# Performance work log

Hardware: AMD Instinct MI355X
Metric: run time of the kernel (lower is better)

## Reference

```python
import jax, jax.numpy as jnp
import numpy as np

B = 128          # batch size
N_KG = 500       # KG vertices
N = N_KG + 2     # + sensor node + zero target node
D = 1024         # embed_dim (hard-coded in forward)
H = 256          # gnn_hidden
E = 4000         # edges
EPS = 1e-5


def setup_inputs() -> dict:
    key = jax.random.key(0)
    ks = jax.random.split(key, 8)
    return {
        "sensor_batch": jax.random.normal(ks[0], (B, D), jnp.float32),
        "base_vertices": jax.random.normal(ks[1], (N_KG, D), jnp.float32),
        "edge_index": jax.random.randint(ks[2], (2, E), 0, N, jnp.int64),
        "W1": jax.random.normal(ks[3], (D, H), jnp.float32) * (1.0 / np.sqrt(D)),
        "b1": jnp.zeros((H,), jnp.float32),
        "gamma1": jnp.ones((H,), jnp.float32),
        "beta1": jnp.zeros((H,), jnp.float32),
        "W2": jax.random.normal(ks[4], (H, H), jnp.float32) * (1.0 / np.sqrt(H)),
        "b2": jnp.zeros((H,), jnp.float32),
        "gamma2": jnp.ones((H,), jnp.float32),
        "beta2": jnp.zeros((H,), jnp.float32),
        "W3": jax.random.normal(ks[5], (H, H), jnp.float32) * (1.0 / np.sqrt(H)),
        "b3": jnp.zeros((H,), jnp.float32),
        "gamma3": jnp.ones((H,), jnp.float32),
        "beta3": jnp.zeros((H,), jnp.float32),
    }


def _gcn_norm(edge_index):
    # add self loops, symmetric normalization D^{-1/2} A D^{-1/2}
    loops = jnp.arange(N, dtype=edge_index.dtype)
    src = jnp.concatenate([edge_index[0], loops])
    dst = jnp.concatenate([edge_index[1], loops])
    deg = jnp.zeros((N,), jnp.float32).at[dst].add(1.0)
    dinv = jnp.where(deg > 0, jax.lax.rsqrt(deg), 0.0)
    norm = dinv[src] * dinv[dst]   # [E+N]
    return src, dst, norm


def _gcn_conv(x, W, b, src, dst, norm):
    # x: [B, N, F_in] -> [B, N, F_out]
    h = jnp.einsum('bnf,fh->bnh', x, W)
    msg = h[:, src, :] * norm[None, :, None]            # gather + scale
    out = jnp.zeros_like(h).at[:, dst, :].add(msg)      # scatter-add
    return out + b


def _bn_elu(x, gamma, beta):
    # BatchNorm1d over flattened (B*N, H) in training mode, then ELU
    Bn, Nn, Hh = x.shape
    xf = x.reshape(Bn * Nn, Hh)
    mean = jnp.mean(xf, axis=0)
    var = jnp.mean(jnp.square(xf - mean), axis=0)  # biased, as in torch BN fwd
    y = (xf - mean) * jax.lax.rsqrt(var + EPS) * gamma + beta
    return jax.nn.elu(y).reshape(Bn, Nn, Hh)


def reference(sensor_batch, base_vertices, edge_index,
              W1, b1, gamma1, beta1,
              W2, b2, gamma2, beta2,
              W3, b3, gamma3, beta3):
    Bn = sensor_batch.shape[0]
    # x = [base_vertices; sensor_input; zeros] per batch element -> [B, N, D]
    base = jnp.broadcast_to(base_vertices[None], (Bn, N_KG, D))
    zeros = jnp.zeros((Bn, 1, D), sensor_batch.dtype)
    x = jnp.concatenate([base, sensor_batch[:, None, :], zeros], axis=1)

    src, dst, norm = _gcn_norm(edge_index)
    x = _bn_elu(_gcn_conv(x, W1, b1, src, dst, norm), gamma1, beta1)
    x = _bn_elu(_gcn_conv(x, W2, b2, src, dst, norm), gamma2, beta2)
    x = _bn_elu(_gcn_conv(x, W3, b3, src, dst, norm), gamma3, beta3)
    return x
```

## Files before the change

kernel.cpp:

```cpp
#include <hip/hip_runtime.h>
#include <cstdint>
#include <cstddef>

#define NNODES 502
#define NKG    500
#define NPAD   512
#define NEDGE  4000
#define NET    4502
#define BB     128
#define DD     1024
#define HH     256
#define MROWS  (BB*NNODES)
#define MT     65536
#define MCAT   628

typedef short short8 __attribute__((ext_vector_type(8)));
typedef float f32x4  __attribute__((ext_vector_type(4)));

__device__ __forceinline__ unsigned short f2bf(float f) {
  union { float f; unsigned int u; } v; v.f = f;
  unsigned int r = v.u + 0x7fffu + ((v.u >> 16) & 1u);
  return (unsigned short)(r >> 16);
}

__device__ __forceinline__ float elu(float y) {
  return (y > 0.f) ? y : (__expf(y) - 1.f);
}

__device__ __forceinline__ void stage16(const void* g, void* l) {
  __builtin_amdgcn_global_load_lds((__attribute__((address_space(1))) void*)g,
                                   (__attribute__((address_space(3))) void*)l, 16, 0, 0);
}

__device__ __forceinline__ void mfma16(f32x4& c, short8 a, short8 b) {
  asm volatile("v_mfma_f32_16x16x32_bf16 %0, %1, %2, %0" : "+v"(c) : "v"(a), "v"(b));
}

__device__ inline void get_edge(const int* __restrict__ e, int i, int i64mode,
                                int& src, int& dst) {
  if (i < NEDGE) {
    if (i64mode) { src = e[2*i]; dst = e[2*NEDGE + 2*i]; }
    else         { src = e[i];   dst = e[NEDGE + i]; }
  } else {
    src = dst = i - NEDGE;
  }
  src = min(max(src, 0), NNODES-1);
  dst = min(max(dst, 0), NNODES-1);
}

__global__ void detect_kernel(const int* __restrict__ e, int* __restrict__ flag) {
  int v = e[2*threadIdx.x + 1];
  if (v != 0) atomicOr(flag, 1);
}

__global__ void deg_kernel(const int* __restrict__ e, const int* __restrict__ flag,
                           int* __restrict__ deg) {
  int i = blockIdx.x*256 + threadIdx.x;
  if (i >= NET) return;
  int src, dst; get_edge(e, i, *flag == 0, src, dst);
  atomicAdd(&deg[dst], 1);
}

__global__ void scan_kernel(const int* __restrict__ deg, float* __restrict__ dinv,
                            int* __restrict__ rp, int* __restrict__ cursor) {
  __shared__ int s[512];
  int t = threadIdx.x;
  int cnt = (t < NNODES) ? deg[t] : 0;
  s[t] = cnt;
  if (t < NNODES) dinv[t] = rsqrtf((float)cnt);
  __syncthreads();
  for (int off = 1; off < 512; off <<= 1) {
    int v = (t >= off) ? s[t-off] : 0;
    __syncthreads();
    s[t] += v;
    __syncthreads();
  }
  if (t == 0) rp[0] = 0;
  if (t < NNODES) { rp[t+1] = s[t]; cursor[t] = s[t] - cnt; }
}

__global__ void fill_kernel(const int* __restrict__ e, const int* __restrict__ flag,
                            const float* __restrict__ dinv, int* __restrict__ cursor,
                            int* __restrict__ colA, float* __restrict__ valA) {
  int i = blockIdx.x*256 + threadIdx.x;
  if (i >= NET) return;
  int src, dst; get_edge(e, i, *flag == 0, src, dst);
  int pos = atomicAdd(&cursor[dst], 1);
  colA[pos] = src;
  valA[pos] = dinv[src] * dinv[dst];
}

__global__ void sdf_kernel(const int* __restrict__ e, const int* __restrict__ flag,
                           const float* __restrict__ dinv, float* __restrict__ Sdf) {
  int i = blockIdx.x*256 + threadIdx.x;
  if (i >= NET) return;
  int src, dst; get_edge(e, i, *flag == 0, src, dst);
  atomicAdd(&Sdf[dst*NPAD + src], dinv[src]*dinv[dst]);
}

__global__ void sdcvt_kernel(const float* __restrict__ Sdf, unsigned short* __restrict__ Sd) {
  int i = blockIdx.x*256 + threadIdx.x;
  Sd[i] = f2bf(Sdf[i]);
}

__global__ __launch_bounds__(256) void prep_kernel(
    const float* __restrict__ W1, const float* __restrict__ W2, const float* __restrict__ W3,
    const float* __restrict__ base, const float* __restrict__ sensor,
    unsigned short* __restrict__ Wt1, unsigned short* __restrict__ Wt2,
    unsigned short* __restrict__ Wt3, unsigned short* __restrict__ Xp1) {
  int bid = blockIdx.x, tid = threadIdx.x;
  if (bid < 512) {
    const float* W = (bid & 256) ? W3 : W2;
    unsigned short* Wt = (bid & 256) ? Wt3 : Wt2;
    int n = bid & 255;
    Wt[n*HH + tid] = f2bf(W[(size_t)tid*HH + n]);
  } else if (bid < 768) {
    int n = bid - 512;
    for (int k = tid; k < DD; k += 256)
      Wt1[n*DD + k] = f2bf(W1[(size_t)k*HH + n]);
  } else {
    int i = (bid - 768)*256 + tid;
    int r = i >> 8, c = (i & 255) * 4;
    float4 v = make_float4(0.f, 0.f, 0.f, 0.f);
    if (r < NKG) v = *(const float4*)&base[(size_t)r*DD + c];
    else if (r < MCAT) v = *(const float4*)&sensor[(size_t)(r-NKG)*DD + c];
    union { unsigned short u[4]; uint2 d; } p;
    p.u[0]=f2bf(v.x); p.u[1]=f2bf(v.y); p.u[2]=f2bf(v.z); p.u[3]=f2bf(v.w);
    *(uint2*)&Xp1[(size_t)r*DD + c] = p.d;
  }
}

__global__ __launch_bounds__(256) void gemm1m_kernel(
    const unsigned short* __restrict__ Ag,
    const unsigned short* __restrict__ Bg,
    float* __restrict__ C) {
  __shared__ unsigned short As[128*32];
  __shared__ unsigned short Bs[128*32];
  int tid = threadIdx.x;
  int wave = tid >> 6, lane = tid & 63;
  int l15 = lane & 15, quad = lane >> 4;
  int wm = (wave & 1) * 64, wn = (wave >> 1) * 64;
  int row0 = blockIdx.y * 128, col0 = blockIdx.x * 128;
  f32x4 acc[4][4] = {};
  for (int k0 = 0; k0 < DD; k0 += 32) {
#pragma unroll
    for (int q = 0; q < 2; ++q) {
      int c = wave*128 + q*64 + lane;
      stage16(Ag + (size_t)(row0 + (c>>2))*DD + k0 + (c&3)*8, As + c*8);
      stage16(Bg + (size_t)(col0 + (c>>2))*DD + k0 + (c&3)*8, Bs + c*8);
    }
    __syncthreads();
    short8 af[4], bfv[4];
#pragma unroll
    for (int i = 0; i < 4; ++i) {
      af[i]  = *(const short8*)(As + (wm + i*16 + l15)*32 + quad*8);
      bfv[i] = *(const short8*)(Bs + (wn + i*16 + l15)*32 + quad*8);
    }
#pragma unroll
    for (int mi = 0; mi < 4; ++mi)
#pragma unroll
      for (int ni = 0; ni < 4; ++ni)
        mfma16(acc[mi][ni], af[mi], bfv[ni]);
    __syncthreads();
  }
  asm volatile("s_nop 7\n\ts_nop 7" ::);
#pragma unroll
  for (int ni = 0; ni < 4; ++ni) {
    int n = col0 + wn + ni*16 + l15;
#pragma unroll
    for (int mi = 0; mi < 4; ++mi) {
      int m = row0 + wm + mi*16 + quad*4;
#pragma unroll
      for (int r = 0; r < 4; ++r)
        if (m + r < MCAT) C[(size_t)(m+r)*HH + n] = acc[mi][ni][r];
    }
  }
}

__global__ void ac_kernel(const int* __restrict__ rp, const int* __restrict__ colA,
                          const float* __restrict__ valA, const float* __restrict__ hcat,
                          float* __restrict__ Abuf, float* __restrict__ cbuf) {
  int n = blockIdx.x, h = threadIdx.x;
  int s = rp[n], e = rp[n+1];
  float acc = 0.f, cacc = 0.f;
  for (int t = s; t < e; ++t) {
    int cl = colA[t]; float v = valA[t];
    if (cl < NKG) acc += v * hcat[cl*HH + h];
    else if (cl == NKG) cacc += v;
  }
  Abuf[n*HH + h] = acc;
  if (h == 0) cbuf[n] = cacc;
}

__global__ __launch_bounds__(256) void bn1n_kernel(
    const float* __restrict__ Abuf, const float* __restrict__ cbuf,
    const float* __restrict__ hcat,
    float* __restrict__ sA1, float* __restrict__ sAA1, float* __restrict__ sAc1,
    float* __restrict__ scp, float* __restrict__ ssA, float* __restrict__ sssA) {
  int bid = blockIdx.x, h = threadIdx.x;
  if (bid < 32) {
    int n0 = bid*16, n1 = min(n0+16, NNODES);
    float sA = 0, sAA = 0, sAc = 0, sc = 0, scc = 0;
    for (int n = n0; n < n1; ++n) {
      float a = Abuf[n*HH + h]; float cn = cbuf[n];
      sA += a; sAA += a*a; sAc += a*cn; sc += cn; scc += cn*cn;
    }
    atomicAdd(&sA1[h], sA); atomicAdd(&sAA1[h], sAA); atomicAdd(&sAc1[h], sAc);
    if (h == 0) { atomicAdd(&scp[0], sc); atomicAdd(&scp[1], scc); }
  } else {
    int b0 = (bid-32)*16;
    float ss = 0, sss = 0;
    for (int b = b0; b < b0+16; ++b) {
      float v = hcat[(size_t)(NKG + b)*HH + h]; ss += v; sss += v*v;
    }
    atomicAdd(&ssA[h], ss); atomicAdd(&sssA[h], sss);
  }
}

__global__ void fin1_kernel(const float* __restrict__ sA1, const float* __restrict__ sAA1,
                            const float* __restrict__ sAc1, const float* __restrict__ scp,
                            const float* __restrict__ ssA, const float* __restrict__ sssA,
                            const float* __restrict__ gamma, const float* __restrict__ beta,
                            float* __restrict__ scale, float* __restrict__ shift) {
  int h = threadIdx.x;
  float sA = sA1[h], sAA = sAA1[h], sAc = sAc1[h];
  float sc = scp[0], scc = scp[1];
  float ss = ssA[h], sss = sssA[h];
  const float cnt = (float)MROWS;
  float mean = ((float)BB * sA + sc*ss) / cnt;
  float msq  = ((float)BB * sAA + 2.f*sAc*ss + scc*sss) / cnt;
  float var  = msq - mean*mean;
  float scl  = gamma[h] * rsqrtf(var + 1e-5f);
  scale[h] = scl; shift[h] = beta[h] - mean*scl;
}

__global__ __launch_bounds__(256) void x2_kernel(
    const float* __restrict__ Abuf, const float* __restrict__ cbuf,
    const float* __restrict__ hcat, const float* __restrict__ scale,
    const float* __restrict__ shift, unsigned short* __restrict__ Xb) {
  int idx = blockIdx.x*256 + threadIdx.x;
  int row = idx >> 6, h0 = (idx & 63)*4;
  int b = row >> 9, n = row & (NPAD-1);
  union { unsigned short u[4]; uint2 d; } p;
  p.d = make_uint2(0,0);
  if (n < NNODES) {
    float4 a  = *(const float4*)(Abuf + n*HH + h0);
    float4 s  = *(const float4*)(hcat + (size_t)(NKG + b)*HH + h0);
    float4 sc = *(const float4*)(scale + h0);
    float4 sh = *(const float4*)(shift + h0);
    float cn = cbuf[n];
    p.u[0] = f2bf(elu((a.x + cn*s.x)*sc.x + sh.x));
    p.u[1] = f2bf(elu((a.y + cn*s.y)*sc.y + sh.y));
    p.u[2] = f2bf(elu((a.z + cn*s.z)*sc.z + sh.z));
    p.u[3] = f2bf(elu((a.w + cn*s.w)*sc.w + sh.w));
  }
  *(uint2*)(Xb + (size_t)row*HH + h0) = p.d;
}

__global__ __launch_bounds__(256) void gemmT_kernel(
    const unsigned short* __restrict__ Ag,
    const unsigned short* __restrict__ Bg,
    unsigned short* __restrict__ Tt) {
  __shared__ unsigned short As[128*32];
  __shared__ unsigned short Bs[128*32];
  int tid = threadIdx.x;
  int wave = tid >> 6, lane = tid & 63;
  int l15 = lane & 15, quad = lane >> 4;
  int wm = (wave & 1) * 64, wn = (wave >> 1) * 64;
  int row0 = blockIdx.y * 128, col0 = blockIdx.x * 128;
  f32x4 acc[4][4] = {};
  for (int k0 = 0; k0 < HH; k0 += 32) {
#pragma unroll
    for (int q = 0; q < 2; ++q) {
      int c = wave*128 + q*64 + lane;
      stage16(Ag + (size_t)(row0 + (c>>2))*HH + k0 + (c&3)*8, As + c*8);
      stage16(Bg + (size_t)(col0 + (c>>2))*HH + k0 + (c&3)*8, Bs + c*8);
    }
    __syncthreads();
    short8 af[4], bfv[4];
#pragma unroll
    for (int i = 0; i < 4; ++i) {
      af[i]  = *(const short8*)(As + (wm + i*16 + l15)*32 + quad*8);
      bfv[i] = *(const short8*)(Bs + (wn + i*16 + l15)*32 + quad*8);
    }
#pragma unroll
    for (int mi = 0; mi < 4; ++mi)
#pragma unroll
      for (int ni = 0; ni < 4; ++ni)
        mfma16(acc[mi][ni], af[mi], bfv[ni]);
    __syncthreads();
  }
  asm volatile("s_nop 7\n\ts_nop 7" ::);
#pragma unroll
  for (int ni = 0; ni < 4; ++ni) {
    int n = col0 + wn + ni*16 + l15;
#pragma unroll
    for (int mi = 0; mi < 4; ++mi) {
      int m = row0 + wm + mi*16 + quad*4;
      union { unsigned short u[4]; uint2 v; } p;
#pragma unroll
      for (int r = 0; r < 4; ++r) p.u[r] = f2bf(acc[mi][ni][r]);
      *(uint2*)(Tt + (size_t)n*MT + m) = p.v;
    }
  }
}

__global__ __launch_bounds__(256) void gemmS_kernel(
    const unsigned short* __restrict__ Sd,
    const unsigned short* __restrict__ Tt,
    float* __restrict__ O,
    float* __restrict__ sums, float* __restrict__ ssqs) {
  __shared__ unsigned short As[128*32];
  __shared__ unsigned short Bs[128*32];
  int tid = threadIdx.x;
  int wave = tid >> 6, lane = tid & 63;
  int l15 = lane & 15, quad = lane >> 4;
  int wm = (wave & 1) * 64, wn = (wave >> 1) * 64;
  int row0 = blockIdx.y * 128, col0 = blockIdx.x * 128;
  int b = blockIdx.z;
  f32x4 acc[4][4] = {};
  for (int k0 = 0; k0 < NPAD; k0 += 32) {
#pragma unroll
    for (int q = 0; q < 2; ++q) {
      int c = wave*128 + q*64 + lane;
      stage16(Sd + (size_t)(row0 + (c>>2))*NPAD + k0 + (c&3)*8, As + c*8);
      stage16(Tt + (size_t)(col0 + (c>>2))*MT + b*NPAD + k0 + (c&3)*8, Bs + c*8);
    }
    __syncthreads();
    short8 af[4], bfv[4];
#pragma unroll
    for (int i = 0; i < 4; ++i) {
      af[i]  = *(const short8*)(As + (wm + i*16 + l15)*32 + quad*8);
      bfv[i] = *(const short8*)(Bs + (wn + i*16 + l15)*32 + quad*8);
    }
#pragma unroll
    for (int mi = 0; mi < 4; ++mi)
#pragma unroll
      for (int ni = 0; ni < 4; ++ni)
        mfma16(acc[mi][ni], af[mi], bfv[ni]);
    __syncthreads();
  }
  asm volatile("s_nop 7\n\ts_nop 7" ::);
  float* Ob = O + (size_t)b*NNODES*HH;
  float ps[4] = {0,0,0,0}, pq[4] = {0,0,0,0};
#pragma unroll
  for (int ni = 0; ni < 4; ++ni) {
    int n = col0 + wn + ni*16 + l15;
#pragma unroll
    for (int mi = 0; mi < 4; ++mi) {
      int node = row0 + wm + mi*16 + quad*4;
#pragma unroll
      for (int r = 0; r < 4; ++r) {
        float v = acc[mi][ni][r];
        if (node + r < NNODES) Ob[(size_t)(node+r)*HH + n] = v;
        ps[ni] += v; pq[ni] += v*v;
      }
    }
  }
  __syncthreads();
  float* red = (float*)As;
  red[tid] = 0.f;
  __syncthreads();
#pragma unroll
  for (int ni = 0; ni < 4; ++ni) {
    int cl = wn + ni*16 + l15;
    atomicAdd(&red[cl], ps[ni]);
    atomicAdd(&red[128+cl], pq[ni]);
  }
  __syncthreads();
  if (tid < 128) atomicAdd(&sums[col0+tid], red[tid]);
  else atomicAdd(&ssqs[col0+tid-128], red[tid]);
}

__global__ void finalize_kernel(const float* __restrict__ sums, const float* __restrict__ ssqs,
                                const float* __restrict__ gamma, const float* __restrict__ beta,
                                float* __restrict__ scale, float* __restrict__ shift) {
  int h = threadIdx.x;
  const float cnt = (float)MROWS;
  float mean = sums[h] / cnt;
  float var  = ssqs[h] / cnt - mean*mean;
  float scl  = gamma[h] * rsqrtf(var + 1e-5f);
  scale[h] = scl; shift[h] = beta[h] - mean*scl;
}

__global__ __launch_bounds__(256) void bnxb_kernel(
    const float* __restrict__ O, const float* __restrict__ scale,
    const float* __restrict__ shift, unsigned short* __restrict__ Xb) {
  int idx = blockIdx.x*256 + threadIdx.x;
  int row = idx >> 6, h0 = (idx & 63)*4;
  int b = row >> 9, n = row & (NPAD-1);
  union { unsigned short u[4]; uint2 d; } p;
  p.d = make_uint2(0,0);
  if (n < NNODES) {
    float4 v  = *(const float4*)(O + ((size_t)(b*NNODES + n)*HH + h0));
    float4 sc = *(const float4*)(scale + h0);
    float4 sh = *(const float4*)(shift + h0);
    p.u[0] = f2bf(elu(v.x*sc.x + sh.x));
    p.u[1] = f2bf(elu(v.y*sc.y + sh.y));
    p.u[2] = f2bf(elu(v.z*sc.z + sh.z));
    p.u[3] = f2bf(elu(v.w*sc.w + sh.w));
  }
  *(uint2*)(Xb + (size_t)row*HH + h0) = p.d;
}

__global__ __launch_bounds__(256) void bnout_kernel(
    float* __restrict__ O, const float* __restrict__ scale,
    const float* __restrict__ shift) {
  int i = blockIdx.x*256 + threadIdx.x;
  int h0 = (i & 63)*4;
  float4 v = *(float4*)(O + (size_t)i*4);
  float4 sc = *(const float4*)(scale + h0);
  float4 sh = *(const float4*)(shift + h0);
  v.x = elu(v.x*sc.x + sh.x);
  v.y = elu(v.y*sc.y + sh.y);
  v.z = elu(v.z*sc.z + sh.z);
  v.w = elu(v.w*sc.w + sh.w);
  *(float4*)(O + (size_t)i*4) = v;
}

extern "C" void kernel_launch(void* const* d_in, const int* in_sizes, int n_in,
                              void* d_out, int out_size, void* d_ws, size_t ws_size,
                              hipStream_t stream) {
  const float* sensor = (const float*)d_in[0];
  const float* base   = (const float*)d_in[1];
  const int*   eidx   = (const int*)d_in[2];
  const float* W1 = (const float*)d_in[3];
  const float* g1 = (const float*)d_in[5];
  const float* be1= (const float*)d_in[6];
  const float* W2 = (const float*)d_in[7];
  const float* g2 = (const float*)d_in[9];
  const float* be2= (const float*)d_in[10];
  const float* W3 = (const float*)d_in[11];
  const float* g3 = (const float*)d_in[13];
  const float* be3= (const float*)d_in[14];

  char* ws = (char*)d_ws;
  int*   deg    = (int*)(ws + 0);
  float* sum2   = (float*)(ws + 2048);
  float* ssq2   = (float*)(ws + 3072);
  float* sum3   = (float*)(ws + 4096);
  float* ssq3   = (float*)(ws + 5120);
  float* cbuf   = (float*)(ws + 6144);
  int*   cursor = (int*)(ws + 8192);
  int*   flag   = (int*)(ws + 10240);
  float* sA1    = (float*)(ws + 10496);
  float* sAA1   = (float*)(ws + 11520);
  float* sAc1   = (float*)(ws + 12544);
  float* scp    = (float*)(ws + 13568);
  float* ssA    = (float*)(ws + 13824);
  float* sssA   = (float*)(ws + 14848);
  float* dinv   = (float*)(ws + 16384);
  int*   rp     = (int*)(ws + 18432);
  int*   colA   = (int*)(ws + 20480);
  float* valA   = (float*)(ws + 40960);
  float* scale1 = (float*)(ws + 61440);
  float* shift1 = (float*)(ws + 62464);
  float* scale2 = (float*)(ws + 63488);
  float* shift2 = (float*)(ws + 64512);
  float* scale3 = (float*)(ws + 65536);
  float* shift3 = (float*)(ws + 66560);
  float* Abuf   = (float*)(ws + 67584);
  float* hcat   = (float*)(ws + 581632);
  unsigned short* Wt2 = (unsigned short*)(ws + 1224704);
  unsigned short* Wt3 = (unsigned short*)(ws + 1355776);
  unsigned short* Sd  = (unsigned short*)(ws + 1486848);
  unsigned short* Xb  = (unsigned short*)(ws + 2011136);
  unsigned short* Tt  = (unsigned short*)(ws + 35565568UL);
  unsigned short* Xp1 = (unsigned short*)(ws + 35565568UL);
  unsigned short* Wt1 = (unsigned short*)(ws + 35565568UL + 1310720);
  float* out = (float*)d_out;
  float* Sdf = (float*)d_out;

  hipMemsetAsync(ws, 0, 16384, stream);
  hipMemsetAsync(d_out, 0, NPAD*NPAD*4, stream);
  detect_kernel<<<1, 256, 0, stream>>>(eidx, flag);
  deg_kernel<<<(NET+255)/256, 256, 0, stream>>>(eidx, flag, deg);
  scan_kernel<<<1, 512, 0, stream>>>(deg, dinv, rp, cursor);
  fill_kernel<<<(NET+255)/256, 256, 0, stream>>>(eidx, flag, dinv, cursor, colA, valA);
  sdf_kernel<<<(NET+255)/256, 256, 0, stream>>>(eidx, flag, dinv, Sdf);
  sdcvt_kernel<<<(NPAD*NPAD)/256, 256, 0, stream>>>(Sdf, Sd);
  prep_kernel<<<1408, 256, 0, stream>>>(W1, W2, W3, base, sensor, Wt1, Wt2, Wt3, Xp1);

  gemm1m_kernel<<<dim3(2, 5), 256, 0, stream>>>(Xp1, Wt1, hcat);
  ac_kernel<<<NNODES, 256, 0, stream>>>(rp, colA, valA, hcat, Abuf, cbuf);
  bn1n_kernel<<<40, 256, 0, stream>>>(Abuf, cbuf, hcat, sA1, sAA1, sAc1, scp, ssA, sssA);
  fin1_kernel<<<1, 256, 0, stream>>>(sA1, sAA1, sAc1, scp, ssA, sssA, g1, be1, scale1, shift1);
  x2_kernel<<<(MT*64)/256, 256, 0, stream>>>(Abuf, cbuf, hcat, scale1, shift1, Xb);

  gemmT_kernel<<<dim3(2, MT/128), 256, 0, stream>>>(Xb, Wt2, Tt);
  gemmS_kernel<<<dim3(2, 4, BB), 256, 0, stream>>>(Sd, Tt, out, sum2, ssq2);
  finalize_kernel<<<1, 256, 0, stream>>>(sum2, ssq2, g2, be2, scale2, shift2);
  bnxb_kernel<<<(MT*64)/256, 256, 0, stream>>>(out, scale2, shift2, Xb);

  gemmT_kernel<<<dim3(2, MT/128), 256, 0, stream>>>(Xb, Wt3, Tt);
  gemmS_kernel<<<dim3(2, 4, BB), 256, 0, stream>>>(Sd, Tt, out, sum3, ssq3);
  finalize_kernel<<<1, 256, 0, stream>>>(sum3, ssq3, g3, be3, scale3, shift3);
  bnout_kernel<<<(MROWS*64)/256, 256, 0, stream>>>(out, scale3, shift3);
}
```

Before: 334.5 us.

## Store aggregation GEMM output as bf16 in place and remap blocks across XCDs

The aggregation GEMM now writes its result as bf16 straight into the activation buffer instead of fp32 into the output. BN+ELU then runs in place on that bf16 buffer, and the final layer converts from bf16 to fp32 output in one pass. This cuts intermediate fp32 traffic. The grid is also flattened to 1D with an XCD-aware index remap so blocks sharing a batch land on the same XCD cache. In exchange, pre-BN values are rounded to bf16 before normalization, which adds some precision loss in the final layer's output.

```diff
diff --git a/kernel.cpp b/kernel.cpp
--- a/kernel.cpp
+++ b/kernel.cpp
@@ -21,6 +21,11 @@
   union { float f; unsigned int u; } v; v.f = f;
   unsigned int r = v.u + 0x7fffu + ((v.u >> 16) & 1u);
   return (unsigned short)(r >> 16);
+}
+
+__device__ __forceinline__ float bf2f(unsigned short u) {
+  union { unsigned int u; float f; } v; v.u = ((unsigned int)u) << 16;
+  return v.f;
 }
 
 __device__ __forceinline__ float elu(float y) {
@@ -308,7 +313,7 @@
 __global__ __launch_bounds__(256) void gemmS_kernel(
     const unsigned short* __restrict__ Sd,
     const unsigned short* __restrict__ Tt,
-    float* __restrict__ O,
+    unsigned short* __restrict__ Xbo,
     float* __restrict__ sums, float* __restrict__ ssqs) {
   __shared__ unsigned short As[128*32];
   __shared__ unsigned short Bs[128*32];
@@ -316,8 +321,14 @@
   int wave = tid >> 6, lane = tid & 63;
   int l15 = lane & 15, quad = lane >> 4;
   int wm = (wave & 1) * 64, wn = (wave >> 1) * 64;
-  int row0 = blockIdx.y * 128, col0 = blockIdx.x * 128;
-  int b = blockIdx.z;
+  int id = blockIdx.x;
+  int xcd = id & 7;
+  int w = id >> 3;
+  int y = w & 3;
+  int g = (w >> 2) * 8 + xcd;
+  int x = g >> 7;
+  int b = g & 127;
+  int row0 = y * 128, col0 = x * 128;
   f32x4 acc[4][4] = {};
   for (int k0 = 0; k0 < NPAD; k0 += 32) {
 #pragma unroll
@@ -341,7 +352,7 @@
     __syncthreads();
   }
   asm volatile("s_nop 7\n\ts_nop 7" ::);
-  float* Ob = O + (size_t)b*NNODES*HH;
+  unsigned short* Xrow = Xbo + (size_t)b*NPAD*HH;
   float ps[4] = {0,0,0,0}, pq[4] = {0,0,0,0};
 #pragma unroll
   for (int ni = 0; ni < 4; ++ni) {
@@ -352,7 +363,7 @@
 #pragma unroll
       for (int r = 0; r < 4; ++r) {
         float v = acc[mi][ni][r];
-        if (node + r < NNODES) Ob[(size_t)(node+r)*HH + n] = v;
+        if (node + r < NNODES) Xrow[(size_t)(node+r)*HH + n] = f2bf(v);
         ps[ni] += v; pq[ni] += v*v;
       }
     }
@@ -383,39 +394,42 @@
   scale[h] = scl; shift[h] = beta[h] - mean*scl;
 }
 
-__global__ __launch_bounds__(256) void bnxb_kernel(
-    const float* __restrict__ O, const float* __restrict__ scale,
-    const float* __restrict__ shift, unsigned short* __restrict__ Xb) {
+__global__ __launch_bounds__(256) void bnip_kernel(
+    unsigned short* __restrict__ Xb, const float* __restrict__ scale,
+    const float* __restrict__ shift) {
+  int idx = blockIdx.x*256 + threadIdx.x;
+  int row = idx >> 6, h0 = (idx & 63)*4;
+  int n = row & (NPAD-1);
+  if (n >= NNODES) return;
+  unsigned short* p = Xb + (size_t)row*HH + h0;
+  union { unsigned short u[4]; uint2 d; } v;
+  v.d = *(uint2*)p;
+  float4 sc = *(const float4*)(scale + h0);
+  float4 sh = *(const float4*)(shift + h0);
+  v.u[0] = f2bf(elu(bf2f(v.u[0])*sc.x + sh.x));
+  v.u[1] = f2bf(elu(bf2f(v.u[1])*sc.y + sh.y));
+  v.u[2] = f2bf(elu(bf2f(v.u[2])*sc.z + sh.z));
+  v.u[3] = f2bf(elu(bf2f(v.u[3])*sc.w + sh.w));
+  *(uint2*)p = v.d;
+}
+
+__global__ __launch_bounds__(256) void bnout_kernel(
+    const unsigned short* __restrict__ Xb, const float* __restrict__ scale,
+    const float* __restrict__ shift, float* __restrict__ O) {
   int idx = blockIdx.x*256 + threadIdx.x;
   int row = idx >> 6, h0 = (idx & 63)*4;
   int b = row >> 9, n = row & (NPAD-1);
-  union { unsigned short u[4]; uint2 d; } p;
-  p.d = make_uint2(0,0);
-  if (n < NNODES) {
-    float4 v  = *(const float4*)(O + ((size_t)(b*NNODES + n)*HH + h0));
-    float4 sc = *(const float4*)(scale + h0);
-    float4 sh = *(const float4*)(shift + h0);
-    p.u[0] = f2bf(elu(v.x*sc.x + sh.x));
-    p.u[1] = f2bf(elu(v.y*sc.y + sh.y));
-    p.u[2] = f2bf(elu(v.z*sc.z + sh.z));
-    p.u[3] = f2bf(elu(v.w*sc.w + sh.w));
-  }
-  *(uint2*)(Xb + (size_t)row*HH + h0) = p.d;
-}
-
-__global__ __launch_bounds__(256) void bnout_kernel(
-    float* __restrict__ O, const float* __restrict__ scale,
-    const float* __restrict__ shift) {
-  int i = blockIdx.x*256 + threadIdx.x;
-  int h0 = (i & 63)*4;
-  float4 v = *(float4*)(O + (size_t)i*4);
+  if (n >= NNODES) return;
+  union { unsigned short u[4]; uint2 d; } v;
+  v.d = *(const uint2*)(Xb + (size_t)row*HH + h0);
   float4 sc = *(const float4*)(scale + h0);
   float4 sh = *(const float4*)(shift + h0);
-  v.x = elu(v.x*sc.x + sh.x);
-  v.y = elu(v.y*sc.y + sh.y);
-  v.z = elu(v.z*sc.z + sh.z);
-  v.w = elu(v.w*sc.w + sh.w);
-  *(float4*)(O + (size_t)i*4) = v;
+  float4 o;
+  o.x = elu(bf2f(v.u[0])*sc.x + sh.x);
+  o.y = elu(bf2f(v.u[1])*sc.y + sh.y);
+  o.z = elu(bf2f(v.u[2])*sc.z + sh.z);
+  o.w = elu(bf2f(v.u[3])*sc.w + sh.w);
+  *(float4*)(O + ((size_t)(b*NNODES + n)*HH + h0)) = o;
 }
 
 extern "C" void kernel_launch(void* const* d_in, const int* in_sizes, int n_in,
@@ -488,12 +502,12 @@
   x2_kernel<<<(MT*64)/256, 256, 0, stream>>>(Abuf, cbuf, hcat, scale1, shift1, Xb);
 
   gemmT_kernel<<<dim3(2, MT/128), 256, 0, stream>>>(Xb, Wt2, Tt);
-  gemmS_kernel<<<dim3(2, 4, BB), 256, 0, stream>>>(Sd, Tt, out, sum2, ssq2);
+  gemmS_kernel<<<1024, 256, 0, stream>>>(Sd, Tt, Xb, sum2, ssq2);
   finalize_kernel<<<1, 256, 0, stream>>>(sum2, ssq2, g2, be2, scale2, shift2);
-  bnxb_kernel<<<(MT*64)/256, 256, 0, stream>>>(out, scale2, shift2, Xb);
+  bnip_kernel<<<(MT*64)/256, 256, 0, stream>>>(Xb, scale2, shift2);
 
   gemmT_kernel<<<dim3(2, MT/128), 256, 0, stream>>>(Xb, Wt3, Tt);
-  gemmS_kernel<<<dim3(2, 4, BB), 256, 0, stream>>>(Sd, Tt, out, sum3, ssq3);
+  gemmS_kernel<<<1024, 256, 0, stream>>>(Sd, Tt, Xb, sum3, ssq3);
   finalize_kernel<<<1, 256, 0, stream>>>(sum3, ssq3, g3, be3, scale3, shift3);
-  bnout_kernel<<<(MROWS*64)/256, 256, 0, stream>>>(out, scale3, shift3);
-}
+  bnout_kernel<<<(MT*64)/256, 256, 0, stream>>>(Xb, scale3, shift3, out);
+}
```

Measured after the change: 328.8 us. No clear change (-1.7%).
